# Kernel tuning notes

Hardware: AMD Instinct MI355X
Metric: run time of the kernel (lower is better)

Reference implementation:

```python
import jax, jax.numpy as jnp
import numpy as np


def _sin_rpe(Lq, d_model, dtype):
    # sinusoidal relative-position embeddings for positions -(Lq-1)..(Lq-1)
    inv_freq = 1.0 / (10000.0 ** (jnp.arange(0, d_model, 2, dtype=jnp.float32) / d_model))
    pos = jnp.arange(-(Lq - 1), Lq, dtype=jnp.float32)  # [2Lq-1]
    ang = pos[:, None] * inv_freq[None, :]               # [2Lq-1, d_model/2]
    emb = jnp.zeros((2 * Lq - 1, d_model), dtype=jnp.float32)
    emb = emb.at[:, 0::2].set(jnp.sin(ang)).at[:, 1::2].set(jnp.cos(ang))
    return emb.astype(dtype)


def _rel_shift(x):
    # Transformer-XL relative shift. x: [B,H,Lq,Lr] with Lr = 2Lq-1
    B, H, Lq, Lr = x.shape
    xp = jnp.concatenate([jnp.zeros((B, H, Lq, 1), x.dtype), x], axis=-1)
    xp = xp.reshape(B, H, Lr + 1, Lq)
    return xp[:, :, 1:].reshape(B, H, Lq, Lr)[..., Lr - Lq:]


def setup_inputs() -> dict:
    key = jax.random.key(0)
    ks = jax.random.split(key, 7)
    B, Lq, D, H = 1, 2048, 1024, 16
    d_head = D // H
    s = 0.02
    return {
        "w": jax.random.normal(ks[0], (B, Lq, D), jnp.float32),
        "Wq": jax.random.normal(ks[1], (D, D), jnp.float32) * s,
        "Wk": jax.random.normal(ks[2], (D, D), jnp.float32) * s,
        "Wv": jax.random.normal(ks[3], (D, D), jnp.float32) * s,
        "Wr": jax.random.normal(ks[4], (D, D), jnp.float32) * s,
        "u_bias": jax.random.normal(ks[5], (H, d_head), jnp.float32) * 0.02,
        "v_bias": jax.random.normal(ks[6], (H, d_head), jnp.float32) * 0.02,
    }


def reference(w, Wq, Wk, Wv, Wr, u_bias, v_bias):
    B, Lq, D = w.shape
    H, d_head = u_bias.shape
    scale = 1.0 / np.sqrt(d_head).astype(np.float32)
    r = _sin_rpe(Lq, D, w.dtype)                          # [2Lq-1, D]
    # torch Linear: y = x @ W.T
    q = (w @ Wq.T).reshape(B, Lq, H, d_head).transpose(0, 2, 1, 3)  # [B,H,Lq,d]
    k = (w @ Wk.T).reshape(B, Lq, H, d_head).transpose(0, 2, 1, 3)
    v = (w @ Wv.T).reshape(B, Lq, H, d_head).transpose(0, 2, 1, 3)
    rp = (r @ Wr.T).reshape(2 * Lq - 1, H, d_head).transpose(1, 0, 2)  # [H,2Lq-1,d]
    AC = jnp.einsum('bhid,bhjd->bhij', q + u_bias[None, :, None, :], k)   # [B,H,Lq,Lq]
    BD = jnp.einsum('bhid,hjd->bhij', q + v_bias[None, :, None, :], rp)   # [B,H,Lq,2Lq-1]
    BD = _rel_shift(BD)                                                   # [B,H,Lq,Lq]
    attn = jax.nn.softmax((AC + BD) * scale, axis=-1)
    out = jnp.einsum('bhij,bhjd->bhid', attn, v)          # [B,H,Lq,d]
    return out.transpose(0, 2, 1, 3).reshape(B, Lq, D)
```

## Files before the change

### kernel.cpp

```cpp
#include <hip/hip_runtime.h>
#include <math.h>
#include <stddef.h>

#define LQ 2048
#define DM 1024
#define NH 16
#define DH 64
#define LR 4095

typedef __attribute__((ext_vector_type(4))) float f4v;
typedef __attribute__((ext_vector_type(8))) short s8v;
typedef __attribute__((ext_vector_type(2))) unsigned short us2;
typedef __attribute__((ext_vector_type(8))) unsigned short us8;
typedef __attribute__((ext_vector_type(2))) unsigned int u32x2;
typedef __attribute__((ext_vector_type(4))) unsigned int u32x4;

__device__ __forceinline__ unsigned short f2bf(float x) {
    unsigned int u = __float_as_uint(x);
    return (unsigned short)((u + 0x7FFFu + ((u >> 16) & 1u)) >> 16);
}
__device__ __forceinline__ float bf2f(unsigned short s) {
    return __uint_as_float(((unsigned int)s) << 16);
}
__device__ __forceinline__ unsigned cvtpk(float lo, float hi) {
    unsigned r;
    asm("v_cvt_pk_bf16_f32 %0, %1, %2" : "=v"(r) : "v"(lo), "v"(hi));
    return r;
}
template<int CTRL>
__device__ __forceinline__ float rot16(float x) {
    return __uint_as_float((unsigned)__builtin_amdgcn_update_dpp(
        0, (int)__float_as_uint(x), CTRL, 0xF, 0xF, false));
}
#define GLOAD16(g, l) __builtin_amdgcn_global_load_lds((g), (l), 16, 0, 0)
#define WAVE_LDS_FENCE() do { \
    asm volatile("s_waitcnt lgkmcnt(0)" ::: "memory"); \
    __builtin_amdgcn_sched_barrier(0); } while (0)

#define MFMA16(a, b, c) __builtin_amdgcn_mfma_f32_16x16x32_bf16((a), (b), (c), 0, 0, 0)

__device__ __forceinline__ s8v sw_read8(const unsigned short* base, int row, int colshort) {
    int byte = (row * 128 + colshort * 2) ^ ((row & 7) << 4);
    return *(const s8v*)((const char*)base + byte);
}

__global__ __launch_bounds__(256)
void prep(const float* __restrict__ w, const float* __restrict__ Wq,
          const float* __restrict__ Wk, const float* __restrict__ Wv,
          const float* __restrict__ Wr, unsigned short* __restrict__ dst,
          unsigned short* __restrict__ r, unsigned short* __restrict__ rpg) {
    int b = blockIdx.x;
    if (b < 3072) {
        size_t e0 = ((size_t)b * 256 + threadIdx.x) * 8;
        const float* src;
        if (e0 < (size_t)LQ * DM) src = w + e0;
        else {
            size_t ro = e0 - (size_t)LQ * DM;
            int wi = (int)(ro >> 20);
            size_t off = ro & 1048575;
            src = (wi == 0 ? Wq : wi == 1 ? Wk : wi == 2 ? Wv : Wr) + off;
        }
        f4v a = *(const f4v*)src;
        f4v c = *(const f4v*)(src + 4);
        us8 o;
        o[0]=f2bf(a[0]); o[1]=f2bf(a[1]); o[2]=f2bf(a[2]); o[3]=f2bf(a[3]);
        o[4]=f2bf(c[0]); o[5]=f2bf(c[1]); o[6]=f2bf(c[2]); o[7]=f2bf(c[3]);
        *(us8*)(dst + e0) = o;
    } else if (b < 11262) {
        int tg = (b - 3072) * 256 + threadIdx.x;
        int gm = tg >> 9, c2 = tg & 511;
        float invf = expf(-(float)c2 * (9.210340371976184f / 512.0f));
        float ang = (float)(gm - (LQ - 1)) * invf;
        float sv, cv;
        sincosf(ang, &sv, &cv);
        us2 o; o[0] = f2bf(sv); o[1] = f2bf(cv);
        *(us2*)&r[(size_t)gm * DM + c2 * 2] = o;
    } else {
        int idx = (b - 11262) * 2048 + threadIdx.x * 8;
        unsigned short* p = (idx < 131072)
            ? (rpg - 131072 + idx)
            : (rpg + (size_t)LR * DM + (idx - 131072));
        *(us8*)p = (us8){0,0,0,0,0,0,0,0};
    }
}

__global__ __launch_bounds__(256, 3)
void proj_all(const unsigned short* __restrict__ wbf, const unsigned short* __restrict__ rr,
              const unsigned short* __restrict__ Wqb, const unsigned short* __restrict__ Wkb,
              const unsigned short* __restrict__ Wvb, const unsigned short* __restrict__ Wrb,
              unsigned short* __restrict__ qb, unsigned short* __restrict__ kkb,
              unsigned short* __restrict__ vtg, unsigned short* __restrict__ rpg) {
    __shared__ unsigned short ldsbuf[2 * 128 * 64];
    unsigned short* As = ldsbuf;
    unsigned short* Bs = ldsbuf + 128 * 64;
    int bid = blockIdx.x;
    int mat, mblk, nblk;
    if (bid < 384) { mat = bid >> 7; int rm = bid & 127; mblk = rm >> 3; nblk = rm & 7; }
    else           { mat = 3; int rm = bid - 384; mblk = rm >> 3; nblk = rm & 7; }
    const int M = (mat < 3) ? LQ : LR;
    const unsigned short* A = (mat < 3) ? wbf : rr;
    const unsigned short* B = mat == 0 ? Wqb : mat == 1 ? Wkb : mat == 2 ? Wvb : Wrb;
    unsigned short* C = mat == 0 ? qb : mat == 1 ? kkb : mat == 2 ? vtg : rpg;
    const int m0 = mblk * 128, n0 = nblk * 128;
    const int t = threadIdx.x;
    const int w = t >> 6, lan16 = t & 15, lgrp = (t & 63) >> 4;
    const int wm = (w >> 1) * 64, wn = (w & 1) * 64;
    f4v acc[4][4] = {};

    for (int k0 = 0; k0 < DM; k0 += 64) {
        #pragma unroll
        for (int it = 0; it < 4; ++it) {
            int slot = it * 256 + t;
            int row = slot >> 3, c8 = slot & 7;
            int gm = m0 + row; if (gm > M - 1) gm = M - 1;
            GLOAD16(A + (size_t)gm * DM + k0 + c8 * 8,
                    (char*)As + (size_t)(it * 256 + (t & ~63)) * 16);
            GLOAD16(B + (size_t)(n0 + row) * DM + k0 + c8 * 8,
                    (char*)Bs + (size_t)(it * 256 + (t & ~63)) * 16);
        }
        __syncthreads();
        #pragma unroll
        for (int kk = 0; kk < 2; ++kk) {
            s8v aF[4], bF[4];
            #pragma unroll
            for (int i = 0; i < 4; ++i) {
                aF[i] = *(const s8v*)&As[(wm + i * 16 + lan16) * 64 + kk * 32 + lgrp * 8];
                bF[i] = *(const s8v*)&Bs[(wn + i * 16 + lan16) * 64 + kk * 32 + lgrp * 8];
            }
            #pragma unroll
            for (int i = 0; i < 4; ++i)
                #pragma unroll
                for (int j = 0; j < 4; ++j)
                    acc[i][j] = MFMA16(aF[i], bF[j], acc[i][j]);
        }
        __syncthreads();
    }
    if (mat != 2) {
        #pragma unroll
        for (int i = 0; i < 4; ++i)
            #pragma unroll
            for (int j = 0; j < 4; ++j)
                #pragma unroll
                for (int rg = 0; rg < 4; ++rg) {
                    int row = m0 + wm + i * 16 + lgrp * 4 + rg;
                    if (row < M)
                        C[(size_t)row * DM + n0 + wn + j * 16 + lan16] = f2bf(acc[i][j][rg]);
                }
    } else {
        unsigned short* Ct = ldsbuf;
        #pragma unroll
        for (int i = 0; i < 4; ++i)
            #pragma unroll
            for (int j = 0; j < 4; ++j) {
                int n = wn + j * 16 + lan16;
                int mb = wm + i * 16 + lgrp * 4;
                int byte = (n * 256 + mb * 2) ^ ((n & 7) << 4);
                u32x2 pp;
                pp[0] = cvtpk(acc[i][j][0], acc[i][j][1]);
                pp[1] = cvtpk(acc[i][j][2], acc[i][j][3]);
                *(u32x2*)((char*)Ct + byte) = pp;
            }
        __syncthreads();
        #pragma unroll
        for (int it = 0; it < 8; ++it) {
            int slot = it * 256 + t;
            int n = slot >> 4, c8 = slot & 15;
            int byte = (n * 256 + c8 * 16) ^ ((n & 7) << 4);
            us8 v = *(const us8*)((const char*)Ct + byte);
            *(us8*)&C[(size_t)(n0 + n) * LQ + m0 + c8 * 8] = v;
        }
    }
}

__global__ __launch_bounds__(256, 2)
void attn_mfma(const unsigned short* __restrict__ q, const unsigned short* __restrict__ kkg,
               const unsigned short* __restrict__ vtg, const unsigned short* __restrict__ rpg,
               const float* __restrict__ ub, const float* __restrict__ vb,
               float* __restrict__ out) {
    __shared__ unsigned short Kb[2][64 * 64];
    __shared__ unsigned short Bb[2][128 * 64];
    __shared__ unsigned short Vb[2][64 * 64];
    __shared__ unsigned short GP[4][80 * 20];

    const int dd = blockIdx.x;
    const int f = (dd & 7) * 64 + (dd >> 3);
    const int h = f >> 5;
    const int i0 = (f & 31) * 64;
    const int col0 = h * DH;

    const int t = threadIdx.x;
    const int w = t >> 6, lan16 = t & 15, lgrp = (t & 63) >> 4;
    const int W = w * 16;
    const int cbase = 48 - W;
    const float C1 = 0.125f * 1.4426950408889634f;
    const float C0 = -4.0f * 1.4426950408889634f;

    unsigned short* gw = GP[w];

    union uv { u32x4 u; s8v s; };
    auto mkfrag = [&](int gi, const float* bias, s8v* dstf) {
        #pragma unroll
        for (int kk = 0; kk < 2; ++kk) {
            int cb = kk * 32 + lgrp * 8;
            us8 qv = (us8){0,0,0,0,0,0,0,0};
            if (gi < LQ) qv = *(const us8*)(q + (size_t)gi * DM + col0 + cb);
            f4v b0 = *(const f4v*)(bias + col0 + cb);
            f4v b1 = *(const f4v*)(bias + col0 + cb + 4);
            uv o;
            o.u[0] = cvtpk(bf2f(qv[0]) + b0[0], bf2f(qv[1]) + b0[1]);
            o.u[1] = cvtpk(bf2f(qv[2]) + b0[2], bf2f(qv[3]) + b0[3]);
            o.u[2] = cvtpk(bf2f(qv[4]) + b1[0], bf2f(qv[5]) + b1[1]);
            o.u[3] = cvtpk(bf2f(qv[6]) + b1[2], bf2f(qv[7]) + b1[3]);
            dstf[kk] = o.s;
        }
    };
    s8v quF[2], qvlF[2], qvsF[2];
    mkfrag(i0 + W + lan16, ub, quF);
    mkfrag(i0 + W + lan16, vb, qvlF);
    mkfrag(i0 + W + 1 + lan16, vb, qvsF);

    auto stageK = [&](int j0, int buf) {
        #pragma unroll
        for (int it = 0; it < 2; ++it) {
            int slot = it * 256 + t;
            int row = slot >> 3, c8 = (t & 7) ^ (row & 7);
            GLOAD16(kkg + (size_t)(j0 + row) * DM + col0 + c8 * 8,
                    (char*)&Kb[buf][0] + (size_t)(it * 256 + (t & ~63)) * 16);
        }
    };
    auto stageB = [&](int rel, int buf) {
        int base = (rel <= 0) ? rel + 4031 : rel - 65;
        #pragma unroll
        for (int it = 0; it < 4; ++it) {
            int slot = it * 256 + t;
            int row = slot >> 3, c8 = (t & 7) ^ (row & 7);
            GLOAD16(rpg + (ptrdiff_t)(base + row) * DM + col0 + c8 * 8,
                    (char*)&Bb[buf][0] + (size_t)(it * 256 + (t & ~63)) * 16);
        }
    };
    auto stageV = [&](int j0, int buf) {
        #pragma unroll
        for (int it = 0; it < 2; ++it) {
            int slot = it * 256 + t;
            int row = slot >> 3, c8 = (t & 7) ^ (row & 7);
            GLOAD16(vtg + (size_t)(col0 + row) * LQ + j0 + c8 * 8,
                    (char*)&Vb[buf][0] + (size_t)(it * 256 + (t & ~63)) * 16);
        }
    };

    f4v accO[4] = {};
    float lsum[4] = {0.f, 0.f, 0.f, 0.f};
    s8v pFprev[2] = {};

    stageK(0, 0);
    stageB(0 - i0, 0);
    stageV(0, 1);
    stageV(0, 0);
    stageK(64, 1);
    stageB(64 - i0, 1);

    auto tile_body = [&](int tt, int cur) {
        const int j0 = tt * 64;
        const int rel = j0 - i0;
        __builtin_amdgcn_sched_barrier(0);
        asm volatile("s_waitcnt vmcnt(8)" ::: "memory");
        __builtin_amdgcn_s_barrier();
        __builtin_amdgcn_sched_barrier(0);

        __builtin_amdgcn_s_setprio(1);
        #pragma unroll
        for (int nf = 0; nf < 4; ++nf)
            #pragma unroll
            for (int kk = 0; kk < 2; ++kk) {
                s8v vF = sw_read8(&Vb[cur ^ 1][0], nf * 16 + lan16, kk * 32 + lgrp * 8);
                accO[nf] = MFMA16(pFprev[kk], vF, accO[nf]);
            }
        f4v acF[4] = {};
        #pragma unroll
        for (int nf = 0; nf < 4; ++nf)
            #pragma unroll
            for (int kk = 0; kk < 2; ++kk) {
                s8v bF = sw_read8(&Kb[cur][0], nf * 16 + lan16, kk * 32 + lgrp * 8);
                acF[nf] = MFMA16(quF[kk], bF, acF[nf]);
            }
        f4v g[5] = {};
        {
            const s8v* qf = (rel <= 0) ? qvlF : qvsF;
            #pragma unroll
            for (int c = 0; c < 5; ++c)
                #pragma unroll
                for (int kk = 0; kk < 2; ++kk) {
                    s8v bF = sw_read8(&Bb[cur][0], cbase + c * 16 + lan16, kk * 32 + lgrp * 8);
                    g[c] = MFMA16(qf[kk], bF, g[c]);
                }
        }
        __builtin_amdgcn_s_setprio(0);
        if (rel == 0) {
            #pragma unroll
            for (int c = 0; c < 5; ++c) {
                int trow = -65 + cbase + c * 16 + lan16;
                const unsigned short* bp = rpg + (ptrdiff_t)trow * DM + col0;
                #pragma unroll
                for (int kk = 0; kk < 2; ++kk) {
                    us8 bv = *(const us8*)(bp + kk * 32 + lgrp * 8);
                    g[c] = MFMA16(qvsF[kk], (s8v)bv, g[c]);
                }
            }
        }
        #pragma unroll
        for (int c = 0; c < 5; ++c) {
            int cl = c * 16 + lan16;
            u32x2 pp;
            pp[0] = cvtpk(g[c][0], g[c][1]);
            pp[1] = cvtpk(g[c][2], g[c][3]);
            *(u32x2*)&gw[cl * 20 + lgrp * 4] = pp;
        }
        WAVE_LDS_FENCE();

        float gval[16];
        #pragma unroll
        for (int nf = 0; nf < 4; ++nf)
            #pragma unroll
            for (int rg = 0; rg < 4; ++rg) {
                const int rhat = lgrp * 4 + rg;
                gval[nf * 4 + rg] = bf2f(gw[(nf * 16 + lan16 - rhat + 15) * 20 + rhat]);
            }
        WAVE_LDS_FENCE();

        #pragma unroll
        for (int nf = 0; nf < 4; ++nf) {
            int jl = nf * 16 + lan16;
            float pp[4];
            #pragma unroll
            for (int rg = 0; rg < 4; ++rg) {
                pp[rg] = exp2f(fmaf(acF[nf][rg] + gval[nf * 4 + rg], C1, C0));
                lsum[rg] += pp[rg];
            }
            u32x2 pk;
            pk[0] = cvtpk(pp[0], pp[1]);
            pk[1] = cvtpk(pp[2], pp[3]);
            *(u32x2*)&gw[jl * 20 + lgrp * 4] = pk;
        }
        WAVE_LDS_FENCE();

        #pragma unroll
        for (int kk = 0; kk < 2; ++kk) {
            us8 tmp;
            #pragma unroll
            for (int e = 0; e < 8; ++e)
                tmp[e] = gw[(kk * 32 + lgrp * 8 + e) * 20 + lan16];
            pFprev[kk] = (s8v)tmp;
        }
        __builtin_amdgcn_sched_barrier(0);
        __builtin_amdgcn_s_barrier();
        __builtin_amdgcn_sched_barrier(0);
        const int tv = (tt < 31) ? tt + 1 : 31;
        const int tn = (tt < 30) ? tt + 2 : 31;
        stageV(tv * 64, cur ^ 1);
        stageK(tn * 64, cur);
        stageB(tn * 64 - i0, cur);
        __builtin_amdgcn_sched_barrier(0);
    };

    #pragma unroll 1
    for (int tp = 0; tp < 16; ++tp) {
        tile_body(tp * 2, 0);
        tile_body(tp * 2 + 1, 1);
    }

    #pragma unroll
    for (int nf = 0; nf < 4; ++nf)
        #pragma unroll
        for (int kk = 0; kk < 2; ++kk) {
            s8v vF = sw_read8(&Vb[1][0], nf * 16 + lan16, kk * 32 + lgrp * 8);
            accO[nf] = MFMA16(pFprev[kk], vF, accO[nf]);
        }

    #pragma unroll
    for (int rg = 0; rg < 4; ++rg) {
        float s = lsum[rg];
        s += rot16<0x121>(s);
        s += rot16<0x122>(s);
        s += rot16<0x124>(s);
        s += rot16<0x128>(s);
        float inv = 1.f / s;
        const int row = i0 + W + lgrp * 4 + rg;
        #pragma unroll
        for (int nf = 0; nf < 4; ++nf)
            out[(size_t)row * DM + col0 + nf * 16 + lan16] = accO[nf][rg] * inv;
    }
}

extern "C" void kernel_launch(void* const* d_in, const int* in_sizes, int n_in,
                              void* d_out, int out_size, void* d_ws, size_t ws_size,
                              hipStream_t stream) {
    const float* w  = (const float*)d_in[0];
    const float* Wq = (const float*)d_in[1];
    const float* Wk = (const float*)d_in[2];
    const float* Wv = (const float*)d_in[3];
    const float* Wr = (const float*)d_in[4];
    const float* ub = (const float*)d_in[5];
    const float* vb = (const float*)d_in[6];
    float* out = (float*)d_out;

    const size_t U = 1048576;
    unsigned short* ws = (unsigned short*)d_ws;
    unsigned short* wbf = ws;
    unsigned short* Wqb = ws + 2 * U;
    unsigned short* Wkb = ws + 3 * U;
    unsigned short* Wvb = ws + 4 * U;
    unsigned short* Wrb = ws + 5 * U;
    unsigned short* qb  = ws + 6 * U;
    unsigned short* kkb = ws + 8 * U;
    unsigned short* vtg = ws + 10 * U;
    unsigned short* rpg = ws + 12 * U + 131072;
    unsigned short* r   = rpg + (size_t)LR * DM + 131072;

    dim3 blk(256);
    hipLaunchKernelGGL(prep, dim3(11390), blk, 0, stream, w, Wq, Wk, Wv, Wr, wbf, r, rpg);
    hipLaunchKernelGGL(proj_all, dim3(640), blk, 0, stream,
                       wbf, r, Wqb, Wkb, Wvb, Wrb, qb, kkb, vtg, rpg);
    hipLaunchKernelGGL(attn_mfma, dim3(512), blk, 0, stream,
                       qb, kkb, vtg, rpg, ub, vb, out);
}
```

Baseline: 119.1 us.

## Transpose MFMA operand order so each lane owns a query row, simplifying LDS shuffles

```diff
diff --git a/kernel.cpp b/kernel.cpp
--- a/kernel.cpp
+++ b/kernel.cpp
@@ -26,11 +26,6 @@
     unsigned r;
     asm("v_cvt_pk_bf16_f32 %0, %1, %2" : "=v"(r) : "v"(lo), "v"(hi));
     return r;
-}
-template<int CTRL>
-__device__ __forceinline__ float rot16(float x) {
-    return __uint_as_float((unsigned)__builtin_amdgcn_update_dpp(
-        0, (int)__float_as_uint(x), CTRL, 0xF, 0xF, false));
 }
 #define GLOAD16(g, l) __builtin_amdgcn_global_load_lds((g), (l), 16, 0, 0)
 #define WAVE_LDS_FENCE() do { \
@@ -180,7 +175,7 @@
     __shared__ unsigned short Kb[2][64 * 64];
     __shared__ unsigned short Bb[2][128 * 64];
     __shared__ unsigned short Vb[2][64 * 64];
-    __shared__ unsigned short GP[4][80 * 20];
+    __shared__ unsigned short GP[4][16 * 84];
 
     const int dd = blockIdx.x;
     const int f = (dd & 7) * 64 + (dd >> 3);
@@ -249,7 +244,7 @@
     };
 
     f4v accO[4] = {};
-    float lsum[4] = {0.f, 0.f, 0.f, 0.f};
+    float lsum = 0.f;
     s8v pFprev[2] = {};
 
     stageK(0, 0);
@@ -273,7 +268,7 @@
             #pragma unroll
             for (int kk = 0; kk < 2; ++kk) {
                 s8v vF = sw_read8(&Vb[cur ^ 1][0], nf * 16 + lan16, kk * 32 + lgrp * 8);
-                accO[nf] = MFMA16(pFprev[kk], vF, accO[nf]);
+                accO[nf] = MFMA16(vF, pFprev[kk], accO[nf]);
             }
         f4v acF[4] = {};
         #pragma unroll
@@ -281,7 +276,7 @@
             #pragma unroll
             for (int kk = 0; kk < 2; ++kk) {
                 s8v bF = sw_read8(&Kb[cur][0], nf * 16 + lan16, kk * 32 + lgrp * 8);
-                acF[nf] = MFMA16(quF[kk], bF, acF[nf]);
+                acF[nf] = MFMA16(bF, quF[kk], acF[nf]);
             }
         f4v g[5] = {};
         {
@@ -291,7 +286,7 @@
                 #pragma unroll
                 for (int kk = 0; kk < 2; ++kk) {
                     s8v bF = sw_read8(&Bb[cur][0], cbase + c * 16 + lan16, kk * 32 + lgrp * 8);
-                    g[c] = MFMA16(qf[kk], bF, g[c]);
+                    g[c] = MFMA16(bF, qf[kk], g[c]);
                 }
         }
         __builtin_amdgcn_s_setprio(0);
@@ -303,17 +298,16 @@
                 #pragma unroll
                 for (int kk = 0; kk < 2; ++kk) {
                     us8 bv = *(const us8*)(bp + kk * 32 + lgrp * 8);
-                    g[c] = MFMA16(qvsF[kk], (s8v)bv, g[c]);
+                    g[c] = MFMA16((s8v)bv, qvsF[kk], g[c]);
                 }
             }
         }
         #pragma unroll
         for (int c = 0; c < 5; ++c) {
-            int cl = c * 16 + lan16;
             u32x2 pp;
             pp[0] = cvtpk(g[c][0], g[c][1]);
             pp[1] = cvtpk(g[c][2], g[c][3]);
-            *(u32x2*)&gw[cl * 20 + lgrp * 4] = pp;
+            *(u32x2*)&gw[lan16 * 84 + c * 16 + lgrp * 4] = pp;
         }
         WAVE_LDS_FENCE();
 
@@ -321,36 +315,28 @@
         #pragma unroll
         for (int nf = 0; nf < 4; ++nf)
             #pragma unroll
+            for (int rg = 0; rg < 4; ++rg)
+                gval[nf * 4 + rg] = bf2f(gw[lan16 * 83 + nf * 16 + lgrp * 4 + rg + 15]);
+        WAVE_LDS_FENCE();
+
+        #pragma unroll
+        for (int nf = 0; nf < 4; ++nf) {
+            float pr[4];
+            #pragma unroll
             for (int rg = 0; rg < 4; ++rg) {
-                const int rhat = lgrp * 4 + rg;
-                gval[nf * 4 + rg] = bf2f(gw[(nf * 16 + lan16 - rhat + 15) * 20 + rhat]);
-            }
+                pr[rg] = exp2f(fmaf(acF[nf][rg] + gval[nf * 4 + rg], C1, C0));
+                lsum += pr[rg];
+            }
+            u32x2 pk;
+            pk[0] = cvtpk(pr[0], pr[1]);
+            pk[1] = cvtpk(pr[2], pr[3]);
+            *(u32x2*)&gw[lan16 * 84 + nf * 16 + lgrp * 4] = pk;
+        }
         WAVE_LDS_FENCE();
 
         #pragma unroll
-        for (int nf = 0; nf < 4; ++nf) {
-            int jl = nf * 16 + lan16;
-            float pp[4];
-            #pragma unroll
-            for (int rg = 0; rg < 4; ++rg) {
-                pp[rg] = exp2f(fmaf(acF[nf][rg] + gval[nf * 4 + rg], C1, C0));
-                lsum[rg] += pp[rg];
-            }
-            u32x2 pk;
-            pk[0] = cvtpk(pp[0], pp[1]);
-            pk[1] = cvtpk(pp[2], pp[3]);
-            *(u32x2*)&gw[jl * 20 + lgrp * 4] = pk;
-        }
-        WAVE_LDS_FENCE();
-
-        #pragma unroll
-        for (int kk = 0; kk < 2; ++kk) {
-            us8 tmp;
-            #pragma unroll
-            for (int e = 0; e < 8; ++e)
-                tmp[e] = gw[(kk * 32 + lgrp * 8 + e) * 20 + lan16];
-            pFprev[kk] = (s8v)tmp;
-        }
+        for (int kk = 0; kk < 2; ++kk)
+            pFprev[kk] = *(const s8v*)&gw[lan16 * 84 + kk * 32 + lgrp * 8];
         __builtin_amdgcn_sched_barrier(0);
         __builtin_amdgcn_s_barrier();
         __builtin_amdgcn_sched_barrier(0);
@@ -368,26 +354,43 @@
         tile_body(tp * 2 + 1, 1);
     }
 
+    asm volatile("s_waitcnt vmcnt(8)" ::: "memory");
     #pragma unroll
     for (int nf = 0; nf < 4; ++nf)
         #pragma unroll
         for (int kk = 0; kk < 2; ++kk) {
             s8v vF = sw_read8(&Vb[1][0], nf * 16 + lan16, kk * 32 + lgrp * 8);
-            accO[nf] = MFMA16(pFprev[kk], vF, accO[nf]);
-        }
-
+            accO[nf] = MFMA16(vF, pFprev[kk], accO[nf]);
+        }
+
+    float s = lsum;
+    s += __shfl_xor(s, 16, 64);
+    s += __shfl_xor(s, 32, 64);
+    float inv = 1.f / s;
+
+    asm volatile("s_waitcnt vmcnt(8)" ::: "memory");
+    __builtin_amdgcn_s_barrier();
+    __builtin_amdgcn_sched_barrier(0);
+    float* Ot = (float*)&Kb[0][0];
+    const int qrow = W + lan16;
     #pragma unroll
-    for (int rg = 0; rg < 4; ++rg) {
-        float s = lsum[rg];
-        s += rot16<0x121>(s);
-        s += rot16<0x122>(s);
-        s += rot16<0x124>(s);
-        s += rot16<0x128>(s);
-        float inv = 1.f / s;
-        const int row = i0 + W + lgrp * 4 + rg;
-        #pragma unroll
-        for (int nf = 0; nf < 4; ++nf)
-            out[(size_t)row * DM + col0 + nf * 16 + lan16] = accO[nf][rg] * inv;
+    for (int nf = 0; nf < 4; ++nf) {
+        f4v ov;
+        #pragma unroll
+        for (int rg = 0; rg < 4; ++rg) ov[rg] = accO[nf][rg] * inv;
+        int byte = (qrow * 256 + (nf * 16 + lgrp * 4) * 4) ^ ((qrow & 7) << 4);
+        *(f4v*)((char*)Ot + byte) = ov;
+    }
+    asm volatile("s_waitcnt lgkmcnt(0)" ::: "memory");
+    __builtin_amdgcn_s_barrier();
+    __builtin_amdgcn_sched_barrier(0);
+    #pragma unroll
+    for (int it = 0; it < 4; ++it) {
+        int idx = it * 256 + t;
+        int row = idx >> 4, ch = idx & 15;
+        int byte = (row * 256 + ch * 16) ^ ((row & 7) << 4);
+        f4v v = *(const f4v*)((const char*)Ot + byte);
+        *(f4v*)&out[(size_t)(i0 + row) * DM + col0 + ch * 4] = v;
     }
 }
 
```

Result: slower. 135.0 us (+13.4%).
